# Performance work log

Measured on AMD Instinct MI355X. Metric: run time of the kernel, lower is better.

## Reference

```python
import jax, jax.numpy as jnp
import numpy as np

EPS = 1e-5
TOP_K = 2


def setup_inputs() -> dict:
    key = jax.random.key(0)
    ks = jax.random.split(key, 6)
    T, H, F, E = 4096, 1024, 2816, 8
    scale = 0.02
    return {
        "hidden_states": jax.random.normal(ks[0], (T, H), dtype=jnp.float32),
        "ln_w": jnp.ones((H,), dtype=jnp.float32),
        "router_w": jax.random.normal(ks[1], (H, E), dtype=jnp.float32) * scale,
        "w_gate": jax.random.normal(ks[2], (E, H, F), dtype=jnp.float32) * scale,
        "w_up": jax.random.normal(ks[3], (E, H, F), dtype=jnp.float32) * scale,
        "w_down": jax.random.normal(ks[4], (E, F, H), dtype=jnp.float32) * scale,
    }


def reference(hidden_states, ln_w, router_w, w_gate, w_up, w_down):
    # RMSNorm (LlamaRMSNorm)
    var = jnp.mean(hidden_states * hidden_states, axis=-1, keepdims=True)
    x = hidden_states * jax.lax.rsqrt(var + EPS) * ln_w  # [T, H]

    # TopKRouter: softmax over experts, then top-k probs/indices
    logits = x @ router_w                     # [T, E]
    probs = jax.nn.softmax(logits, axis=-1)
    topk_p, topk_i = jax.lax.top_k(probs, TOP_K)  # [T, K]

    # Dense combine weights [T, E]: prob for routed experts, 0 otherwise
    T = x.shape[0]
    combine = jnp.zeros_like(probs).at[jnp.arange(T)[:, None], topk_i].add(topk_p)

    # Experts: Llama-style gated MLP (SwiGLU); loop over fixed small expert set
    out = jnp.zeros_like(x)
    for e in range(w_gate.shape[0]):
        h = jax.nn.silu(x @ w_gate[e]) * (x @ w_up[e])   # [T, F]
        out = out + combine[:, e:e + 1] * (h @ w_down[e])
    return out
```

## Files before the change

kernel.cpp:

```cpp
#include <hip/hip_runtime.h>

#define T_TOK 4096
#define H_DIM 1024
#define F_DIM 2816
#define E_NUM 8
#define EPSV 1e-5f

typedef unsigned short u16;
typedef __attribute__((ext_vector_type(8))) short bf16x8;
typedef __attribute__((ext_vector_type(16))) float f32x16;
typedef __attribute__((ext_vector_type(8))) u16 u16x8;

__device__ __forceinline__ u16 f2bf(float f) {
  union { float f; unsigned u; } c; c.f = f;
  unsigned u = c.u;
  return (u16)((u + 0x7FFFu + ((u >> 16) & 1u)) >> 16);
}

__device__ __forceinline__ void llds16(const u16* g, u16* l) {
  __builtin_amdgcn_global_load_lds(
      (const __attribute__((address_space(1))) unsigned int*)g,
      (__attribute__((address_space(3))) unsigned int*)l, 16, 0, 0);
}

__global__ __launch_bounds__(256) void router_kernel(
    const float* __restrict__ hs, const float* __restrict__ lnw,
    const float* __restrict__ rw, u16* __restrict__ x_h,
    int* __restrict__ cnt, int* __restrict__ list,
    float* __restrict__ wcomb) {
  const int wave = threadIdx.x >> 6;
  const int lane = threadIdx.x & 63;
  const int t = blockIdx.x * 4 + wave;
  const float* row = hs + (size_t)t * H_DIM;

  float4 v[4];
  float ss = 0.f;
#pragma unroll
  for (int j = 0; j < 4; ++j) {
    v[j] = ((const float4*)row)[j * 64 + lane];
    ss += v[j].x * v[j].x + v[j].y * v[j].y + v[j].z * v[j].z + v[j].w * v[j].w;
  }
#pragma unroll
  for (int m = 32; m; m >>= 1) ss += __shfl_xor(ss, m, 64);
  const float inv = rsqrtf(ss * (1.0f / H_DIM) + EPSV);

  float lg[E_NUM];
#pragma unroll
  for (int e = 0; e < E_NUM; ++e) lg[e] = 0.f;

#pragma unroll
  for (int j = 0; j < 4; ++j) {
    const int idx = j * 64 + lane;
    const int h0 = idx * 4;
    float4 w4 = ((const float4*)lnw)[idx];
    float xv[4] = {v[j].x * inv * w4.x, v[j].y * inv * w4.y,
                   v[j].z * inv * w4.z, v[j].w * inv * w4.w};
    ushort4 xs;
    xs.x = f2bf(xv[0]); xs.y = f2bf(xv[1]); xs.z = f2bf(xv[2]); xs.w = f2bf(xv[3]);
    ((ushort4*)(x_h + (size_t)t * H_DIM))[idx] = xs;
#pragma unroll
    for (int q = 0; q < 4; ++q) {
      const float* rr = rw + (size_t)(h0 + q) * E_NUM;
      float4 a = ((const float4*)rr)[0];
      float4 b = ((const float4*)rr)[1];
      lg[0] += xv[q] * a.x; lg[1] += xv[q] * a.y;
      lg[2] += xv[q] * a.z; lg[3] += xv[q] * a.w;
      lg[4] += xv[q] * b.x; lg[5] += xv[q] * b.y;
      lg[6] += xv[q] * b.z; lg[7] += xv[q] * b.w;
    }
  }
#pragma unroll
  for (int e = 0; e < E_NUM; ++e)
#pragma unroll
    for (int m = 32; m; m >>= 1) lg[e] += __shfl_xor(lg[e], m, 64);

  if (lane == 0) {
    float mx = lg[0];
#pragma unroll
    for (int e = 1; e < E_NUM; ++e) mx = fmaxf(mx, lg[e]);
    float p[E_NUM], s = 0.f;
#pragma unroll
    for (int e = 0; e < E_NUM; ++e) { p[e] = __expf(lg[e] - mx); s += p[e]; }
    const float invs = 1.0f / s;
    int e1 = 0; float b1 = p[0];
#pragma unroll
    for (int e = 1; e < E_NUM; ++e) if (p[e] > b1) { b1 = p[e]; e1 = e; }
    int e2 = -1; float b2 = -1.f;
#pragma unroll
    for (int e = 0; e < E_NUM; ++e) if (e != e1 && p[e] > b2) { b2 = p[e]; e2 = e; }
    b1 *= invs; b2 *= invs;
    int p1 = atomicAdd(&cnt[e1], 1);
    list[e1 * T_TOK + p1] = t; wcomb[e1 * T_TOK + p1] = b1;
    int p2 = atomicAdd(&cnt[e2], 1);
    list[e2 * T_TOK + p2] = t; wcomb[e2 * T_TOK + p2] = b2;
  }
}

__global__ void offsets_kernel(const int* __restrict__ cnt, int* __restrict__ offs) {
  if (threadIdx.x == 0) {
    int s = 0;
    for (int e = 0; e < E_NUM; ++e) { offs[e] = s; s += cnt[e]; }
  }
}

__global__ __launch_bounds__(256) void transpose_fused(
    const float* __restrict__ wg, const float* __restrict__ wu,
    const float* __restrict__ wd, u16* __restrict__ wgT,
    u16* __restrict__ wuT, u16* __restrict__ wdT) {
  __shared__ float tile[64 * 65];
  const int bid = blockIdx.x;
  const int seg = bid / 5632;
  const int rem = bid - seg * 5632;
  const int e = rem / 704;
  const int tt = rem - e * 704;
  int R, C, rt, ct;
  const float* in; u16* outp;
  if (seg < 2) {
    R = H_DIM; C = F_DIM; rt = tt / 44; ct = tt - rt * 44;
    in = seg ? wu : wg; outp = seg ? wuT : wgT;
  } else {
    R = F_DIM; C = H_DIM; rt = tt / 16; ct = tt - rt * 16;
    in = wd; outp = wdT;
  }
  const size_t base = (size_t)e * R * C;
  const int r0 = rt * 64, c0 = ct * 64;
  const int tid = threadIdx.x;
  const int rr = tid >> 4, cv = tid & 15;
#pragma unroll
  for (int p = 0; p < 4; ++p) {
    int r = p * 16 + rr;
    float4 v = *(const float4*)(in + base + (size_t)(r0 + r) * C + c0 + cv * 4);
    tile[r * 65 + cv * 4 + 0] = v.x;
    tile[r * 65 + cv * 4 + 1] = v.y;
    tile[r * 65 + cv * 4 + 2] = v.z;
    tile[r * 65 + cv * 4 + 3] = v.w;
  }
  __syncthreads();
#pragma unroll
  for (int q = 0; q < 2; ++q) {
    int id = q * 256 + tid;
    int c = id >> 3, rc = id & 7;
    u16x8 o;
#pragma unroll
    for (int j = 0; j < 8; ++j) o[j] = f2bf(tile[(rc * 8 + j) * 65 + c]);
    *(u16x8*)(outp + base + (size_t)(c0 + c) * R + r0 + rc * 8) = o;
  }
}

__global__ __launch_bounds__(256) void gemm1_kernel(
    const u16* __restrict__ x_h, const u16* __restrict__ wgT,
    const u16* __restrict__ wuT, const int* __restrict__ cnt,
    const int* __restrict__ offs, const int* __restrict__ list,
    u16* __restrict__ hbuf) {
  const int e = blockIdx.z;
  const int n_e = cnt[e];
  const int rt = blockIdx.y;
  if (rt * 128 >= n_e) return;
  const int ft = blockIdx.x;

  __shared__ __align__(16) u16 As[128 * 64];
  __shared__ __align__(16) u16 Bgs[128 * 64];
  __shared__ __align__(16) u16 Bus[128 * 64];
  __shared__ int tok[128];

  const int tid = threadIdx.x;
  if (tid < 128) {
    int r = rt * 128 + tid;
    if (r >= n_e) r = n_e - 1;
    tok[tid] = list[e * T_TOK + r];
  }
  __syncthreads();

  const int wv = tid >> 6, lane = tid & 63;
  const int wm = wv >> 1, wn = wv & 1;
  const int l31 = lane & 31, kh = lane >> 5, l7 = lane & 7;
  const int sr = lane >> 3;
  const int sw = (l7 ^ sr) << 3;

  const size_t wb = ((size_t)e * F_DIM + (size_t)ft * 128) * H_DIM;
  const u16* agp[4]; const u16* bgp[4]; const u16* bup[4];
#pragma unroll
  for (int i = 0; i < 4; ++i) {
    int r = wv * 32 + i * 8 + sr;
    agp[i] = x_h + (size_t)tok[r] * H_DIM + sw;
    bgp[i] = wgT + wb + (size_t)r * H_DIM + sw;
    bup[i] = wuT + wb + (size_t)r * H_DIM + sw;
  }

  int arow[2], brow[2];
#pragma unroll
  for (int t = 0; t < 2; ++t) {
    arow[t] = (wm * 64 + t * 32 + l31) * 64;
    brow[t] = (wn * 64 + t * 32 + l31) * 64;
  }

  f32x16 accg[2][2], accu[2][2];
#pragma unroll
  for (int i = 0; i < 2; ++i)
#pragma unroll
    for (int j = 0; j < 2; ++j) {
      accg[i][j] = (f32x16)(0.f);
      accu[i][j] = (f32x16)(0.f);
    }

  for (int k0 = 0; k0 < H_DIM; k0 += 64) {
#pragma unroll
    for (int i = 0; i < 4; ++i) {
      llds16(agp[i] + k0, &As[(wv * 32 + i * 8) * 64]);
      llds16(bgp[i] + k0, &Bgs[(wv * 32 + i * 8) * 64]);
      llds16(bup[i] + k0, &Bus[(wv * 32 + i * 8) * 64]);
    }
    __syncthreads();
#pragma unroll
    for (int ks = 0; ks < 4; ++ks) {
      const int cho = (((ks * 2) | kh) ^ l7) << 3;
      bf16x8 a[2], bg[2], bu[2];
#pragma unroll
      for (int t = 0; t < 2; ++t) {
        a[t]  = *(const bf16x8*)&As [arow[t] + cho];
        bg[t] = *(const bf16x8*)&Bgs[brow[t] + cho];
        bu[t] = *(const bf16x8*)&Bus[brow[t] + cho];
      }
#pragma unroll
      for (int tm = 0; tm < 2; ++tm)
#pragma unroll
        for (int tn = 0; tn < 2; ++tn) {
          accg[tm][tn] = __builtin_amdgcn_mfma_f32_32x32x16_bf16(a[tm], bg[tn], accg[tm][tn], 0, 0, 0);
          accu[tm][tn] = __builtin_amdgcn_mfma_f32_32x32x16_bf16(a[tm], bu[tn], accu[tm][tn], 0, 0, 0);
        }
    }
    __syncthreads();
  }

  const int oe = offs[e];
#pragma unroll
  for (int tm = 0; tm < 2; ++tm)
#pragma unroll
    for (int rg = 0; rg < 16; ++rg) {
      const int rowi = (rg & 3) + 8 * (rg >> 2) + 4 * kh;
      const int gr = rt * 128 + wm * 64 + tm * 32 + rowi;
      if (gr < n_e) {
        const size_t ob = (size_t)(oe + gr) * F_DIM + ft * 128 + wn * 64 + l31;
#pragma unroll
        for (int tn = 0; tn < 2; ++tn) {
          float g = accg[tm][tn][rg];
          float u = accu[tm][tn][rg];
          float hv = g / (1.0f + __expf(-g)) * u;
          hbuf[ob + tn * 32] = f2bf(hv);
        }
      }
    }
}

__global__ __launch_bounds__(256) void gemm2_kernel(
    const u16* __restrict__ hbuf, const u16* __restrict__ wdT,
    const int* __restrict__ cnt, const int* __restrict__ offs,
    const int* __restrict__ list, const float* __restrict__ wcomb,
    float* __restrict__ out) {
  const int e = blockIdx.z;
  const int n_e = cnt[e];
  const int rt = blockIdx.y;
  if (rt * 128 >= n_e) return;
  const int nt = blockIdx.x;

  __shared__ __align__(16) u16 As[128 * 64];
  __shared__ __align__(16) u16 Bs[128 * 64];
  __shared__ int hrow[128];

  const int tid = threadIdx.x;
  const int oe = offs[e];
  if (tid < 128) {
    int r = rt * 128 + tid;
    if (r >= n_e) r = n_e - 1;
    hrow[tid] = oe + r;
  }
  __syncthreads();

  const int wv = tid >> 6, lane = tid & 63;
  const int wm = wv >> 1, wn = wv & 1;
  const int l31 = lane & 31, kh = lane >> 5, l7 = lane & 7;
  const int sr = lane >> 3;
  const int sw = (l7 ^ sr) << 3;

  const size_t wb = ((size_t)e * H_DIM + (size_t)nt * 128) * F_DIM;
  const u16* agp[4]; const u16* bgp[4];
#pragma unroll
  for (int i = 0; i < 4; ++i) {
    int r = wv * 32 + i * 8 + sr;
    agp[i] = hbuf + (size_t)hrow[r] * F_DIM + sw;
    bgp[i] = wdT + wb + (size_t)r * F_DIM + sw;
  }

  int arow[2], brow[2];
#pragma unroll
  for (int t = 0; t < 2; ++t) {
    arow[t] = (wm * 64 + t * 32 + l31) * 64;
    brow[t] = (wn * 64 + t * 32 + l31) * 64;
  }

  f32x16 acc[2][2];
#pragma unroll
  for (int i = 0; i < 2; ++i)
#pragma unroll
    for (int j = 0; j < 2; ++j) acc[i][j] = (f32x16)(0.f);

  for (int k0 = 0; k0 < F_DIM; k0 += 64) {
#pragma unroll
    for (int i = 0; i < 4; ++i) {
      llds16(agp[i] + k0, &As[(wv * 32 + i * 8) * 64]);
      llds16(bgp[i] + k0, &Bs[(wv * 32 + i * 8) * 64]);
    }
    __syncthreads();
#pragma unroll
    for (int ks = 0; ks < 4; ++ks) {
      const int cho = (((ks * 2) | kh) ^ l7) << 3;
      bf16x8 a[2], b[2];
#pragma unroll
      for (int t = 0; t < 2; ++t) {
        a[t] = *(const bf16x8*)&As[arow[t] + cho];
        b[t] = *(const bf16x8*)&Bs[brow[t] + cho];
      }
#pragma unroll
      for (int tm = 0; tm < 2; ++tm)
#pragma unroll
        for (int tn = 0; tn < 2; ++tn)
          acc[tm][tn] = __builtin_amdgcn_mfma_f32_32x32x16_bf16(a[tm], b[tn], acc[tm][tn], 0, 0, 0);
    }
    __syncthreads();
  }

#pragma unroll
  for (int tm = 0; tm < 2; ++tm)
#pragma unroll
    for (int rg = 0; rg < 16; ++rg) {
      const int rowi = (rg & 3) + 8 * (rg >> 2) + 4 * kh;
      const int gr = rt * 128 + wm * 64 + tm * 32 + rowi;
      if (gr < n_e) {
        const int t = list[e * T_TOK + gr];
        const float cw = wcomb[e * T_TOK + gr];
        float* ob = out + (size_t)t * H_DIM + nt * 128 + wn * 64 + l31;
#pragma unroll
        for (int tn = 0; tn < 2; ++tn)
          atomicAdd(ob + tn * 32, acc[tm][tn][rg] * cw);
      }
    }
}

extern "C" void kernel_launch(void* const* d_in, const int* in_sizes, int n_in,
                              void* d_out, int out_size, void* d_ws, size_t ws_size,
                              hipStream_t stream) {
  const float* hs  = (const float*)d_in[0];
  const float* lnw = (const float*)d_in[1];
  const float* rw  = (const float*)d_in[2];
  const float* wg  = (const float*)d_in[3];
  const float* wu  = (const float*)d_in[4];
  const float* wd  = (const float*)d_in[5];
  float* out = (float*)d_out;

  char* p = (char*)d_ws;
  const size_t SZ_XH = (size_t)T_TOK * H_DIM * 2;
  const size_t SZ_W  = (size_t)E_NUM * F_DIM * H_DIM * 2;
  const size_t SZ_HB = (size_t)T_TOK * 2 * F_DIM * 2;

  u16* x_h  = (u16*)p;   p += SZ_XH;
  u16* wgT  = (u16*)p;   p += SZ_W;
  u16* wuT  = (u16*)p;   p += SZ_W;
  u16* wdT  = (u16*)p;   p += SZ_W;
  u16* hbuf = (u16*)p;   p += SZ_HB;
  int* cnt  = (int*)p;   p += 256;
  int* offs = (int*)p;   p += 256;
  int* list = (int*)p;   p += (size_t)E_NUM * T_TOK * 4;
  float* wcomb = (float*)p; p += (size_t)E_NUM * T_TOK * 4;

  hipMemsetAsync(cnt, 0, 256, stream);
  hipMemsetAsync(out, 0, (size_t)out_size * 4, stream);
  router_kernel<<<T_TOK / 4, 256, 0, stream>>>(hs, lnw, rw, x_h, cnt, list, wcomb);
  offsets_kernel<<<1, 64, 0, stream>>>(cnt, offs);
  transpose_fused<<<3 * 5632, 256, 0, stream>>>(wg, wu, wd, wgT, wuT, wdT);
  gemm1_kernel<<<dim3(F_DIM / 128, T_TOK / 128, E_NUM), 256, 0, stream>>>(x_h, wgT, wuT, cnt, offs, list, hbuf);
  gemm2_kernel<<<dim3(H_DIM / 128, T_TOK / 128, E_NUM), 256, 0, stream>>>(hbuf, wdT, cnt, offs, list, wcomb, out);
}
```

Measured before the change: 725.3 us.

## Split fused gate/up GEMM into two passes and replace atomics with combine

Result: faster. 686.4 us (-5.4%).

```diff
diff --git a/kernel.cpp b/kernel.cpp
--- a/kernel.cpp
+++ b/kernel.cpp
@@ -16,6 +16,10 @@
   unsigned u = c.u;
   return (u16)((u + 0x7FFFu + ((u >> 16) & 1u)) >> 16);
 }
+__device__ __forceinline__ float bf2f(u16 h) {
+  union { unsigned u; float f; } c; c.u = (unsigned)h << 16;
+  return c.f;
+}
 
 __device__ __forceinline__ void llds16(const u16* g, u16* l) {
   __builtin_amdgcn_global_load_lds(
@@ -27,7 +31,7 @@
     const float* __restrict__ hs, const float* __restrict__ lnw,
     const float* __restrict__ rw, u16* __restrict__ x_h,
     int* __restrict__ cnt, int* __restrict__ list,
-    float* __restrict__ wcomb) {
+    float* __restrict__ wcomb, int* __restrict__ slot) {
   const int wave = threadIdx.x >> 6;
   const int lane = threadIdx.x & 63;
   const int t = blockIdx.x * 4 + wave;
@@ -91,8 +95,10 @@
     b1 *= invs; b2 *= invs;
     int p1 = atomicAdd(&cnt[e1], 1);
     list[e1 * T_TOK + p1] = t; wcomb[e1 * T_TOK + p1] = b1;
+    slot[2 * t] = (e1 << 16) | p1;
     int p2 = atomicAdd(&cnt[e2], 1);
     list[e2 * T_TOK + p2] = t; wcomb[e2 * T_TOK + p2] = b2;
+    slot[2 * t + 1] = (e2 << 16) | p2;
   }
 }
 
@@ -147,11 +153,11 @@
   }
 }
 
-__global__ __launch_bounds__(256) void gemm1_kernel(
-    const u16* __restrict__ x_h, const u16* __restrict__ wgT,
-    const u16* __restrict__ wuT, const int* __restrict__ cnt,
+__global__ __launch_bounds__(256, 3) void gemm1_pass(
+    const u16* __restrict__ xs, const u16* __restrict__ wT,
+    const u16* __restrict__ gin, const int* __restrict__ cnt,
     const int* __restrict__ offs, const int* __restrict__ list,
-    u16* __restrict__ hbuf) {
+    u16* __restrict__ outb, int fuse) {
   const int e = blockIdx.z;
   const int n_e = cnt[e];
   const int rt = blockIdx.y;
@@ -159,8 +165,7 @@
   const int ft = blockIdx.x;
 
   __shared__ __align__(16) u16 As[128 * 64];
-  __shared__ __align__(16) u16 Bgs[128 * 64];
-  __shared__ __align__(16) u16 Bus[128 * 64];
+  __shared__ __align__(16) u16 Bs[128 * 64];
   __shared__ int tok[128];
 
   const int tid = threadIdx.x;
@@ -178,13 +183,12 @@
   const int sw = (l7 ^ sr) << 3;
 
   const size_t wb = ((size_t)e * F_DIM + (size_t)ft * 128) * H_DIM;
-  const u16* agp[4]; const u16* bgp[4]; const u16* bup[4];
+  const u16* agp[4]; const u16* bgp[4];
 #pragma unroll
   for (int i = 0; i < 4; ++i) {
     int r = wv * 32 + i * 8 + sr;
-    agp[i] = x_h + (size_t)tok[r] * H_DIM + sw;
-    bgp[i] = wgT + wb + (size_t)r * H_DIM + sw;
-    bup[i] = wuT + wb + (size_t)r * H_DIM + sw;
+    agp[i] = xs + (size_t)tok[r] * H_DIM + sw;
+    bgp[i] = wT + wb + (size_t)r * H_DIM + sw;
   }
 
   int arow[2], brow[2];
@@ -194,40 +198,33 @@
     brow[t] = (wn * 64 + t * 32 + l31) * 64;
   }
 
-  f32x16 accg[2][2], accu[2][2];
+  f32x16 acc[2][2];
 #pragma unroll
   for (int i = 0; i < 2; ++i)
 #pragma unroll
-    for (int j = 0; j < 2; ++j) {
-      accg[i][j] = (f32x16)(0.f);
-      accu[i][j] = (f32x16)(0.f);
-    }
+    for (int j = 0; j < 2; ++j) acc[i][j] = (f32x16)(0.f);
 
   for (int k0 = 0; k0 < H_DIM; k0 += 64) {
 #pragma unroll
     for (int i = 0; i < 4; ++i) {
       llds16(agp[i] + k0, &As[(wv * 32 + i * 8) * 64]);
-      llds16(bgp[i] + k0, &Bgs[(wv * 32 + i * 8) * 64]);
-      llds16(bup[i] + k0, &Bus[(wv * 32 + i * 8) * 64]);
+      llds16(bgp[i] + k0, &Bs[(wv * 32 + i * 8) * 64]);
     }
     __syncthreads();
 #pragma unroll
     for (int ks = 0; ks < 4; ++ks) {
       const int cho = (((ks * 2) | kh) ^ l7) << 3;
-      bf16x8 a[2], bg[2], bu[2];
+      bf16x8 a[2], b[2];
 #pragma unroll
       for (int t = 0; t < 2; ++t) {
-        a[t]  = *(const bf16x8*)&As [arow[t] + cho];
-        bg[t] = *(const bf16x8*)&Bgs[brow[t] + cho];
-        bu[t] = *(const bf16x8*)&Bus[brow[t] + cho];
+        a[t] = *(const bf16x8*)&As[arow[t] + cho];
+        b[t] = *(const bf16x8*)&Bs[brow[t] + cho];
       }
 #pragma unroll
       for (int tm = 0; tm < 2; ++tm)
 #pragma unroll
-        for (int tn = 0; tn < 2; ++tn) {
-          accg[tm][tn] = __builtin_amdgcn_mfma_f32_32x32x16_bf16(a[tm], bg[tn], accg[tm][tn], 0, 0, 0);
-          accu[tm][tn] = __builtin_amdgcn_mfma_f32_32x32x16_bf16(a[tm], bu[tn], accu[tm][tn], 0, 0, 0);
-        }
+        for (int tn = 0; tn < 2; ++tn)
+          acc[tm][tn] = __builtin_amdgcn_mfma_f32_32x32x16_bf16(a[tm], b[tn], acc[tm][tn], 0, 0, 0);
     }
     __syncthreads();
   }
@@ -243,20 +240,21 @@
         const size_t ob = (size_t)(oe + gr) * F_DIM + ft * 128 + wn * 64 + l31;
 #pragma unroll
         for (int tn = 0; tn < 2; ++tn) {
-          float g = accg[tm][tn][rg];
-          float u = accu[tm][tn][rg];
-          float hv = g / (1.0f + __expf(-g)) * u;
-          hbuf[ob + tn * 32] = f2bf(hv);
+          float v = acc[tm][tn][rg];
+          if (fuse) {
+            float g = bf2f(gin[ob + tn * 32]);
+            v = g / (1.0f + __expf(-g)) * v;
+          }
+          outb[ob + tn * 32] = f2bf(v);
         }
       }
     }
 }
 
-__global__ __launch_bounds__(256) void gemm2_kernel(
+__global__ __launch_bounds__(256, 3) void gemm2_kernel(
     const u16* __restrict__ hbuf, const u16* __restrict__ wdT,
     const int* __restrict__ cnt, const int* __restrict__ offs,
-    const int* __restrict__ list, const float* __restrict__ wcomb,
-    float* __restrict__ out) {
+    const float* __restrict__ wcomb, float* __restrict__ contrib) {
   const int e = blockIdx.z;
   const int n_e = cnt[e];
   const int rt = blockIdx.y;
@@ -336,14 +334,26 @@
       const int rowi = (rg & 3) + 8 * (rg >> 2) + 4 * kh;
       const int gr = rt * 128 + wm * 64 + tm * 32 + rowi;
       if (gr < n_e) {
-        const int t = list[e * T_TOK + gr];
         const float cw = wcomb[e * T_TOK + gr];
-        float* ob = out + (size_t)t * H_DIM + nt * 128 + wn * 64 + l31;
+        const size_t ob = (size_t)(oe + gr) * H_DIM + nt * 128 + wn * 64 + l31;
 #pragma unroll
         for (int tn = 0; tn < 2; ++tn)
-          atomicAdd(ob + tn * 32, acc[tm][tn][rg] * cw);
+          contrib[ob + tn * 32] = acc[tm][tn][rg] * cw;
       }
     }
+}
+
+__global__ __launch_bounds__(256) void combine_kernel(
+    const float* __restrict__ contrib, const int* __restrict__ offs,
+    const int* __restrict__ slot, float* __restrict__ out) {
+  const int t = blockIdx.x;
+  const int s0 = slot[2 * t], s1 = slot[2 * t + 1];
+  const int r0 = offs[s0 >> 16] + (s0 & 0xFFFF);
+  const int r1 = offs[s1 >> 16] + (s1 & 0xFFFF);
+  float4 a = ((const float4*)(contrib + (size_t)r0 * H_DIM))[threadIdx.x];
+  float4 b = ((const float4*)(contrib + (size_t)r1 * H_DIM))[threadIdx.x];
+  float4 o = {a.x + b.x, a.y + b.y, a.z + b.z, a.w + b.w};
+  ((float4*)(out + (size_t)t * H_DIM))[threadIdx.x] = o;
 }
 
 extern "C" void kernel_launch(void* const* d_in, const int* in_sizes, int n_in,
@@ -366,17 +376,24 @@
   u16* wgT  = (u16*)p;   p += SZ_W;
   u16* wuT  = (u16*)p;   p += SZ_W;
   u16* wdT  = (u16*)p;   p += SZ_W;
+  u16* gbuf = (u16*)p;   p += SZ_HB;
   u16* hbuf = (u16*)p;   p += SZ_HB;
   int* cnt  = (int*)p;   p += 256;
   int* offs = (int*)p;   p += 256;
   int* list = (int*)p;   p += (size_t)E_NUM * T_TOK * 4;
   float* wcomb = (float*)p; p += (size_t)E_NUM * T_TOK * 4;
+  int* slot = (int*)p;   p += (size_t)T_TOK * 2 * 4;
+  float* contrib = (float*)wgT;
 
   hipMemsetAsync(cnt, 0, 256, stream);
-  hipMemsetAsync(out, 0, (size_t)out_size * 4, stream);
-  router_kernel<<<T_TOK / 4, 256, 0, stream>>>(hs, lnw, rw, x_h, cnt, list, wcomb);
+  router_kernel<<<T_TOK / 4, 256, 0, stream>>>(hs, lnw, rw, x_h, cnt, list, wcomb, slot);
   offsets_kernel<<<1, 64, 0, stream>>>(cnt, offs);
   transpose_fused<<<3 * 5632, 256, 0, stream>>>(wg, wu, wd, wgT, wuT, wdT);
-  gemm1_kernel<<<dim3(F_DIM / 128, T_TOK / 128, E_NUM), 256, 0, stream>>>(x_h, wgT, wuT, cnt, offs, list, hbuf);
-  gemm2_kernel<<<dim3(H_DIM / 128, T_TOK / 128, E_NUM), 256, 0, stream>>>(hbuf, wdT, cnt, offs, list, wcomb, out);
-}
+  gemm1_pass<<<dim3(F_DIM / 128, T_TOK / 128, E_NUM), 256, 0, stream>>>(
+      x_h, wgT, (const u16*)nullptr, cnt, offs, list, gbuf, 0);
+  gemm1_pass<<<dim3(F_DIM / 128, T_TOK / 128, E_NUM), 256, 0, stream>>>(
+      x_h, wuT, gbuf, cnt, offs, list, hbuf, 1);
+  gemm2_kernel<<<dim3(H_DIM / 128, T_TOK / 128, E_NUM), 256, 0, stream>>>(
+      hbuf, wdT, cnt, offs, wcomb, contrib);
+  combine_kernel<<<T_TOK, 256, 0, stream>>>(contrib, offs, slot, out);
+}
```
